# Kernel tuning notes

Measured on AMD Instinct MI355X. Metric: run time of the kernel, lower is better.

The kernel has to match this reference:

```python
import jax, jax.numpy as jnp
import numpy as np

B, S, D, H = 64, 256, 2048, 16
HD = D // H  # 128
MAXS = 256


def setup_inputs() -> dict:
    key = jax.random.key(0)
    ks = jax.random.split(key, 16)
    sc = 0.02
    inp = {
        "q": jax.random.normal(ks[0], (B, S, D), jnp.float32),
        "k": jax.random.normal(ks[1], (B, S, D), jnp.float32),
        "v": jax.random.normal(ks[2], (B, S, D), jnp.float32),
        "attention_mask": jax.random.randint(ks[3], (B, S), 0, 2, jnp.int32),
        # projection weights, torch Linear convention: y = x @ W.T + b
        "Wq": jax.random.normal(ks[4], (D, D), jnp.float32) * sc,
        "bq": jnp.zeros((D,), jnp.float32),
        "Wk": jax.random.normal(ks[5], (D, D), jnp.float32) * sc,
        "bk": jnp.zeros((D,), jnp.float32),
        "Wv": jax.random.normal(ks[6], (D, D), jnp.float32) * sc,
        "bv": jnp.zeros((D,), jnp.float32),
        "Wo": jax.random.normal(ks[7], (D, D), jnp.float32) * sc,
        "bo": jnp.zeros((D,), jnp.float32),
        # additive per-head bias table (max_sequence_length=256)
        "bias_table": jax.random.normal(ks[8], (H, MAXS, MAXS), jnp.float32) * 0.1,
    }
    return inp


def reference(q, k, v, attention_mask, Wq, bq, Wk, bk, Wv, bv, Wo, bo, bias_table):
    def proj(x, W, b):  # (B,S,D) -> (B,H,S,HD)
        y = x @ W.T + b
        return y.reshape(B, S, H, HD).transpose(0, 2, 1, 3)

    qh = proj(q, Wq, bq)
    kh = proj(k, Wk, bk)
    vh = proj(v, Wv, bv)

    # (B,H,Sq,Sk) scores
    scores = jnp.einsum("bhqd,bhkd->bhqk", qh, kh) / jnp.sqrt(jnp.float32(HD))
    scores = scores + bias_table[None, :, :S, :S]
    # mask: (B,Sk) -> (B,1,1,Sk); masked_fill where mask==0
    neg_inf = jnp.finfo(scores.dtype).min
    scores = jnp.where(attention_mask[:, None, None, :] == 0, neg_inf, scores)
    probs = jax.nn.softmax(scores, axis=-1)  # dropout p=0.0 -> identity
    out = jnp.einsum("bhqk,bhkd->bhqd", probs, vh)
    out = out.transpose(0, 2, 1, 3).reshape(B, S, D)
    return out @ Wo.T + bo
```

## Files before the change

### kernel.cpp

```cpp
#include <hip/hip_runtime.h>
#include <hip/hip_bf16.h>

typedef __attribute__((ext_vector_type(4))) float f32x4;
typedef __attribute__((ext_vector_type(8))) short s16x8;
typedef __attribute__((ext_vector_type(4))) unsigned short u16x4;
typedef __attribute__((ext_vector_type(8))) unsigned short u16x8;
typedef __attribute__((ext_vector_type(4))) int i32x4;

#define NB 64
#define NS 256
#define ND 2048
#define NH 16
#define NHD 128

__device__ __forceinline__ unsigned short f2bf(float f){
  unsigned int u = __float_as_uint(f);
  u += 0x7fffu + ((u >> 16) & 1u);
  return (unsigned short)(u >> 16);
}

__device__ __forceinline__ void gload16(const void* g, void* l){
  __builtin_amdgcn_global_load_lds(
    (const __attribute__((address_space(1))) unsigned int*)g,
    (__attribute__((address_space(3))) unsigned int*)l, 16, 0, 0);
}

#define SBAR()  __builtin_amdgcn_sched_barrier(0)
#define BARRIER() do{ SBAR(); __builtin_amdgcn_s_barrier(); SBAR(); }while(0)
#define WAIT_LGKM0() do{ asm volatile("s_waitcnt lgkmcnt(0)" ::: "memory"); SBAR(); }while(0)
#define WAIT_VM0()   do{ asm volatile("s_waitcnt vmcnt(0)"   ::: "memory"); SBAR(); }while(0)
#define WAIT_VM4()   do{ asm volatile("s_waitcnt vmcnt(4)"   ::: "memory"); SBAR(); }while(0)
#define WAIT_VM8()   do{ asm volatile("s_waitcnt vmcnt(8)"   ::: "memory"); SBAR(); }while(0)

__global__ __launch_bounds__(256) void wconv(const float* __restrict__ s,
                                             unsigned short* __restrict__ d, int n8){
  int i = blockIdx.x*256 + threadIdx.x;
  if (i >= n8) return;
  f32x4 a = *(const f32x4*)(s + (size_t)i*8);
  f32x4 b = *(const f32x4*)(s + (size_t)i*8 + 4);
  u16x8 u;
  #pragma unroll
  for (int r=0;r<4;r++){ u[r]=f2bf(a[r]); u[4+r]=f2bf(b[r]); }
  *(u16x8*)(d + (size_t)i*8) = u;
}

template<int OUTMODE>
__global__ __launch_bounds__(512, 2) void gemm256(
    const unsigned short* __restrict__ A, const unsigned short* __restrict__ Bw,
    const float* __restrict__ bias, void* __restrict__ Out, int m_base)
{
  extern __shared__ __attribute__((aligned(16))) char ldsb[];
  const int tid  = threadIdx.x;
  const int lane = tid & 63, wid = tid >> 6;
  const int g = lane >> 4, l15 = lane & 15;
  const int wm = wid >> 2, wn = wid & 3;

  const int nwg = gridDim.x, bid = blockIdx.x;
  const int swz = (bid & 7) * (nwg >> 3) + (bid >> 3);
  const int mt = swz >> 3, nt = swz & 7;
  const int m0 = mt*256, n0 = nt*256;

  const int srow_l = tid >> 3;
  const int scol   = (((tid & 7) ^ (srow_l & 7)) * 8);
  const unsigned short* gsrc[4];
  gsrc[0] = A  + (size_t)(m0 +       srow_l)*ND + scol;
  gsrc[1] = A  + (size_t)(m0 + 128 + srow_l)*ND + scol;
  gsrc[2] = Bw + (size_t)(n0 +       srow_l)*ND + scol;
  gsrc[3] = Bw + (size_t)(n0 + 128 + srow_l)*ND + scol;

#define STAGE(buf, p, kt) do{ \
    const unsigned short* s_ = gsrc[p] + (kt); \
    char* d_ = ldsb + (buf)*65536 + ((p)>>1)*32768 + ((p)&1)*16384 + tid*16; \
    gload16(s_, d_); gload16(s_ + (size_t)64*ND, d_ + 8192); }while(0)

#define RD_A(buf, qa) do{ \
    _Pragma("unroll") for (int i_=0;i_<4;i_++){ \
      int hr = (qa)*64 + i_*16 + l15; \
      const char* p_ = ldsb + (buf)*65536 + wm*16384 + hr*128; \
      _Pragma("unroll") for (int ks_=0;ks_<2;ks_++) \
        av[i_][ks_] = *(const s16x8*)(p_ + (((ks_*4+g) ^ (hr&7))*16)); } }while(0)

#define RD_B(buf, dst, qb) do{ \
    _Pragma("unroll") for (int j_=0;j_<2;j_++){ \
      int hc = (wn&1)*64 + (qb)*32 + j_*16 + l15; \
      const char* p_ = ldsb + (buf)*65536 + 32768 + (wn>>1)*16384 + hc*128; \
      _Pragma("unroll") for (int ks_=0;ks_<2;ks_++) \
        dst[j_][ks_] = *(const s16x8*)(p_ + (((ks_*4+g) ^ (hc&7))*16)); } }while(0)

#define MFMA_PH(qa, qb, bv) do{ \
    __builtin_amdgcn_s_setprio(1); \
    _Pragma("unroll") for (int i_=0;i_<4;i_++) \
      _Pragma("unroll") for (int j_=0;j_<2;j_++) \
        _Pragma("unroll") for (int ks_=0;ks_<2;ks_++) \
          acc[(qa)*4+i_][(qb)*2+j_] = __builtin_amdgcn_mfma_f32_16x16x32_bf16( \
              av[i_][ks_], bv[j_][ks_], acc[(qa)*4+i_][(qb)*2+j_], 0,0,0); \
    __builtin_amdgcn_s_setprio(0); }while(0)

#define HALF(d, ktA, ktB, wmode) do{ \
    RD_A(d,0); RD_B(d,bva,0); \
    if ((ktA)>=0) STAGE((d)^1, 0, ktA); \
    BARRIER(); WAIT_LGKM0(); \
    MFMA_PH(0,0,bva); \
    BARRIER(); \
    RD_B(d,bvb,1); \
    if ((ktA)>=0) STAGE((d)^1, 1, ktA); \
    BARRIER(); WAIT_LGKM0(); \
    MFMA_PH(0,1,bvb); \
    BARRIER(); \
    RD_A(d,1); \
    if ((ktB)>=0) STAGE(d, 2, ktB); \
    BARRIER(); WAIT_LGKM0(); \
    MFMA_PH(1,0,bva); \
    BARRIER(); \
    if ((ktB)>=0) STAGE(d, 3, ktB); \
    MFMA_PH(1,1,bvb); \
    if ((wmode)==0){ WAIT_VM4(); BARRIER(); } \
    else if ((wmode)==1){ WAIT_VM0(); BARRIER(); } \
  }while(0)

  f32x4 acc[8][4];
  s16x8 av[4][2], bva[2][2], bvb[2][2];

  STAGE(0,0,0); STAGE(0,1,0); STAGE(0,2,0); STAGE(0,3,0);
  STAGE(1,2,64); STAGE(1,3,64);
  #pragma unroll
  for (int i=0;i<8;i++)
    #pragma unroll
    for (int j=0;j<4;j++) acc[i][j] = f32x4{0.f,0.f,0.f,0.f};
  WAIT_VM4();
  BARRIER();

  for (int t = 0; t < 15; ++t) {
    HALF(0, (2*t+1)*64, (2*t+2)*64, 0);
    HALF(1, (2*t+2)*64, (2*t+3)*64, 0);
  }
  HALF(0, 31*64, -1, 1);
  HALF(1, -1, -1, -1);

  #pragma unroll
  for (int jx=0;jx<4;jx++){
    int n = n0 + wn*64 + ((jx>>1)<<5) + ((jx&1)<<4) + l15;
    float bj = bias[n];
    #pragma unroll
    for (int i=0;i<8;i++){
      int mb = m_base + m0 + wm*128 + ((i>>2)<<6) + ((i&3)<<4) + g*4;
      if (OUTMODE == 2){
        float* O = (float*)Out;
        #pragma unroll
        for (int r=0;r<4;r++) O[(size_t)(mb+r)*ND + n] = acc[i][jx][r] + bj;
      } else if (OUTMODE == 0){
        unsigned short* O = (unsigned short*)Out;
        int bb = mb >> 8, h = n >> 7, d = n & 127, s0 = mb & 255;
        #pragma unroll
        for (int r=0;r<4;r++)
          O[(((size_t)bb*NH + h)*NS + s0 + r)*NHD + d] = f2bf(acc[i][jx][r] + bj);
      } else {
        unsigned short* O = (unsigned short*)Out;
        int bb = mb >> 8, h = n >> 7, d = n & 127, s0 = mb & 255;
        u16x4 u;
        #pragma unroll
        for (int r=0;r<4;r++) u[r] = f2bf(acc[i][jx][r] + bj);
        *(u16x4*)(O + (((size_t)bb*NH + h)*NHD + d)*NS + s0) = u;
      }
    }
  }
#undef STAGE
#undef RD_A
#undef RD_B
#undef MFMA_PH
#undef HALF
}

__global__ __launch_bounds__(512, 1) void attn_fused2(
  const unsigned short* __restrict__ Qh, const unsigned short* __restrict__ Kh,
  const unsigned short* __restrict__ VT, const int* __restrict__ mask,
  const float* __restrict__ bias_table, unsigned short* __restrict__ AO)
{
  __shared__ unsigned short Klds[256*128];
  __shared__ unsigned short Vlds[128*256];
  char* Kb_ = (char*)Klds; char* Vb_ = (char*)Vlds;
  const int bh = blockIdx.x, b = bh >> 4, h = bh & 15;
  const int tid = threadIdx.x, lane = tid & 63, w = tid >> 6;
  const int g = lane >> 4, l15 = lane & 15;

  {
    const unsigned short* Ksrc = Kh + (size_t)bh*NS*NHD;
    int r0 = tid >> 4, sl = tid & 15;
    #pragma unroll
    for (int c=0;c<8;c++){
      int row = c*32 + r0;
      gload16(Ksrc + (size_t)row*NHD + ((sl ^ (row&7))*8), Kb_ + c*8192 + tid*16);
    }
  }
  {
    const unsigned short* Vsrc = VT + (size_t)bh*NHD*NS;
    int r0 = tid >> 5, sl = tid & 31;
    #pragma unroll
    for (int c=0;c<8;c++){
      int row = c*16 + r0;
      gload16(Vsrc + (size_t)row*NS + ((sl ^ (row&7))*8), Vb_ + c*8192 + tid*16);
    }
  }
  WAIT_VM8();
  BARRIER();

  const float scale = 0.08838834764831845f;
  const int* mrow = mask + b*NS;
  const int s0l = l15 + ((g&1)<<5), s1l = s0l + 16;
  const int sel = g >> 1;

  auto pass = [&](int p, bool wait_v){
    const int q = w*32 + p*16 + l15;
    const unsigned short* Qrow = Qh + ((size_t)bh*NS + q)*NHD;
    s16x8 bq[4];
    #pragma unroll
    for (int kk=0;kk<4;kk++) bq[kk] = *(const s16x8*)(Qrow + kk*32 + g*8);

    f32x4 c[16];
    __builtin_amdgcn_s_setprio(1);
    #pragma unroll
    for (int kb=0;kb<16;kb++){
      c[kb] = f32x4{0.f,0.f,0.f,0.f};
      int row = kb*16 + l15;
      #pragma unroll
      for (int kk=0;kk<4;kk++){
        s16x8 a = *(const s16x8*)(Kb_ + row*256 + (((kk*4+g) ^ (row&7))*16));
        c[kb] = __builtin_amdgcn_mfma_f32_16x16x32_bf16(a, bq[kk], c[kb], 0,0,0);
      }
    }
    __builtin_amdgcn_s_setprio(0);

    const float* brow = bias_table + ((size_t)h*NS + q)*NS;
    float mx = -3.0e38f;
    #pragma unroll
    for (int kb=0;kb<16;kb++){
      f32x4 b4 = *(const f32x4*)(brow + kb*16 + g*4);
      i32x4 m4 = *(const i32x4*)(mrow + kb*16 + g*4);
      #pragma unroll
      for (int r=0;r<4;r++){
        float val = (m4[r] != 0) ? (c[kb][r]*scale + b4[r]) : -3.0e38f;
        c[kb][r] = val;
        mx = fmaxf(mx, val);
      }
    }
    mx = fmaxf(mx, __shfl_xor(mx, 16));
    mx = fmaxf(mx, __shfl_xor(mx, 32));
    float sum = 0.f;
    #pragma unroll
    for (int kb=0;kb<16;kb++)
      #pragma unroll
      for (int r=0;r<4;r++){
        float pv = __expf(c[kb][r] - mx);
        c[kb][r] = pv; sum += pv;
      }
    sum += __shfl_xor(sum, 16);
    sum += __shfl_xor(sum, 32);
    float inv = 1.f / sum;

    unsigned int pk[16][2];
    #pragma unroll
    for (int kb=0;kb<16;kb++){
      pk[kb][0] = (unsigned int)f2bf(c[kb][0]*inv) | ((unsigned int)f2bf(c[kb][1]*inv) << 16);
      pk[kb][1] = (unsigned int)f2bf(c[kb][2]*inv) | ((unsigned int)f2bf(c[kb][3]*inv) << 16);
    }

    if (wait_v){ WAIT_VM0(); BARRIER(); }

    s16x8 pb[8];
    #pragma unroll
    for (int kk=0;kk<8;kk++){
      unsigned int e0 = (unsigned int)__shfl((int)pk[2*kk][0],   s0l);
      unsigned int e1 = (unsigned int)__shfl((int)pk[2*kk][1],   s0l);
      unsigned int e2 = (unsigned int)__shfl((int)pk[2*kk][0],   s1l);
      unsigned int e3 = (unsigned int)__shfl((int)pk[2*kk][1],   s1l);
      unsigned int o0 = (unsigned int)__shfl((int)pk[2*kk+1][0], s0l);
      unsigned int o1 = (unsigned int)__shfl((int)pk[2*kk+1][1], s0l);
      unsigned int o2 = (unsigned int)__shfl((int)pk[2*kk+1][0], s1l);
      unsigned int o3 = (unsigned int)__shfl((int)pk[2*kk+1][1], s1l);
      union { unsigned int wd[4]; s16x8 v; } u_;
      u_.wd[0] = sel ? o0 : e0; u_.wd[1] = sel ? o1 : e1;
      u_.wd[2] = sel ? o2 : e2; u_.wd[3] = sel ? o3 : e3;
      pb[kk] = u_.v;
    }

    f32x4 oacc[8];
    __builtin_amdgcn_s_setprio(1);
    #pragma unroll
    for (int dt=0;dt<8;dt++){
      oacc[dt] = f32x4{0.f,0.f,0.f,0.f};
      int row = dt*16 + l15;
      #pragma unroll
      for (int kk=0;kk<8;kk++){
        s16x8 a = *(const s16x8*)(Vb_ + row*512 + (((kk*4+g) ^ (row&7))*16));
        oacc[dt] = __builtin_amdgcn_mfma_f32_16x16x32_bf16(a, pb[kk], oacc[dt], 0,0,0);
      }
    }
    __builtin_amdgcn_s_setprio(0);

    #pragma unroll
    for (int dt=0;dt<8;dt++){
      u16x4 u;
      #pragma unroll
      for (int r=0;r<4;r++) u[r] = f2bf(oacc[dt][r]);
      *(u16x4*)(AO + ((size_t)b*NS + q)*ND + h*NHD + dt*16 + g*4) = u;
    }
  };

  pass(0, true);
  pass(1, false);
}

extern "C" void kernel_launch(void* const* d_in, const int* in_sizes, int n_in,
                              void* d_out, int out_size, void* d_ws, size_t ws_size,
                              hipStream_t stream)
{
  const float* q  = (const float*)d_in[0];
  const float* k  = (const float*)d_in[1];
  const float* v  = (const float*)d_in[2];
  const int* mask = (const int*)d_in[3];
  const float* Wq = (const float*)d_in[4];
  const float* bq = (const float*)d_in[5];
  const float* Wk = (const float*)d_in[6];
  const float* bk = (const float*)d_in[7];
  const float* Wv = (const float*)d_in[8];
  const float* bv = (const float*)d_in[9];
  const float* Wo = (const float*)d_in[10];
  const float* bo = (const float*)d_in[11];
  const float* bias_table = (const float*)d_in[12];

  char* ws = (char*)d_ws;
  unsigned short* Wob = (unsigned short*)(ws + 0);
  unsigned short* wb  = (unsigned short*)(ws + 8388608);
  unsigned short* tmp = (unsigned short*)(ws + 16777216);
  unsigned short* Qh  = (unsigned short*)(ws + 83886080);
  unsigned short* Kh  = (unsigned short*)(ws + 150994944);
  unsigned short* VT  = (unsigned short*)(ws + 218103808);
  unsigned short* AO  = (unsigned short*)(ws + 285212672);

  hipFuncSetAttribute((const void*)gemm256<0>, hipFuncAttributeMaxDynamicSharedMemorySize, 131072);
  hipFuncSetAttribute((const void*)gemm256<1>, hipFuncAttributeMaxDynamicSharedMemorySize, 131072);
  hipFuncSetAttribute((const void*)gemm256<2>, hipFuncAttributeMaxDynamicSharedMemorySize, 131072);

  wconv<<<2048,256,0,stream>>>(Wo, Wob, 524288);

  const float* acts[3]  = {q, k, v};
  const float* wgt[3]   = {Wq, Wk, Wv};
  const float* bia[3]   = {bq, bk, bv};
  unsigned short* outs[3] = {Qh, Kh, VT};

  for (int x = 0; x < 3; ++x) {
    wconv<<<2048,256,0,stream>>>(wgt[x], wb, 524288);
    wconv<<<16384,256,0,stream>>>(acts[x], tmp, 4194304);
    if (x < 2)
      gemm256<0><<<512,512,131072,stream>>>(tmp, wb, bia[x], outs[x], 0);
    else
      gemm256<1><<<512,512,131072,stream>>>(tmp, wb, bia[x], outs[x], 0);
  }

  attn_fused2<<<1024,512,0,stream>>>(Qh,Kh,VT,mask,bias_table,AO);
  gemm256<2><<<512,512,131072,stream>>>(AO,Wob,bo,(float*)d_out,0);
}
```

Before: 745.6 us.

## Fuse fp32-to-bf16 activation conversion into the QKV projection GEMM loads

Adds a GEMM variant that loads fp32 activations straight into registers, converts them to bf16 and writes them to LDS inside the software pipeline, replacing the separate activation conversion kernels and their scratch buffer. This removes three full-size fp32 read plus bf16 write/read round trips through memory. In exchange the A-operand staging now goes through registers rather than direct global-to-LDS loads, which raises register pressure and adds conversion ALU work inside the main loop. Weight conversions are also hoisted into four back-to-back launches up front.

```diff
diff --git a/kernel.cpp b/kernel.cpp
--- a/kernel.cpp
+++ b/kernel.cpp
@@ -44,34 +44,17 @@
   *(u16x8*)(d + (size_t)i*8) = u;
 }
 
-template<int OUTMODE>
-__global__ __launch_bounds__(512, 2) void gemm256(
-    const unsigned short* __restrict__ A, const unsigned short* __restrict__ Bw,
-    const float* __restrict__ bias, void* __restrict__ Out, int m_base)
-{
-  extern __shared__ __attribute__((aligned(16))) char ldsb[];
-  const int tid  = threadIdx.x;
-  const int lane = tid & 63, wid = tid >> 6;
-  const int g = lane >> 4, l15 = lane & 15;
-  const int wm = wid >> 2, wn = wid & 3;
-
-  const int nwg = gridDim.x, bid = blockIdx.x;
-  const int swz = (bid & 7) * (nwg >> 3) + (bid >> 3);
-  const int mt = swz >> 3, nt = swz & 7;
-  const int m0 = mt*256, n0 = nt*256;
-
-  const int srow_l = tid >> 3;
-  const int scol   = (((tid & 7) ^ (srow_l & 7)) * 8);
-  const unsigned short* gsrc[4];
-  gsrc[0] = A  + (size_t)(m0 +       srow_l)*ND + scol;
-  gsrc[1] = A  + (size_t)(m0 + 128 + srow_l)*ND + scol;
-  gsrc[2] = Bw + (size_t)(n0 +       srow_l)*ND + scol;
-  gsrc[3] = Bw + (size_t)(n0 + 128 + srow_l)*ND + scol;
-
-#define STAGE(buf, p, kt) do{ \
-    const unsigned short* s_ = gsrc[p] + (kt); \
-    char* d_ = ldsb + (buf)*65536 + ((p)>>1)*32768 + ((p)&1)*16384 + tid*16; \
-    gload16(s_, d_); gload16(s_ + (size_t)64*ND, d_ + 8192); }while(0)
+#define GEMM_COMMON_DECLS \
+  extern __shared__ __attribute__((aligned(16))) char ldsb[]; \
+  const int tid  = threadIdx.x; \
+  const int lane = tid & 63, wid = tid >> 6; \
+  const int g = lane >> 4, l15 = lane & 15; \
+  const int wm = wid >> 2, wn = wid & 3; \
+  const int nwg = gridDim.x, bid = blockIdx.x; \
+  const int swz = (bid & 7) * (nwg >> 3) + (bid >> 3); \
+  const int mt = swz >> 3, nt = swz & 7; \
+  const int m0 = mt*256, n0 = nt*256; \
+  const int srow_l = tid >> 3, slot = tid & 7;
 
 #define RD_A(buf, qa) do{ \
     _Pragma("unroll") for (int i_=0;i_<4;i_++){ \
@@ -96,6 +79,50 @@
               av[i_][ks_], bv[j_][ks_], acc[(qa)*4+i_][(qb)*2+j_], 0,0,0); \
     __builtin_amdgcn_s_setprio(0); }while(0)
 
+#define GEMM_EPILOGUE(OUTMODE_) \
+  _Pragma("unroll") \
+  for (int jx=0;jx<4;jx++){ \
+    int n = n0 + wn*64 + ((jx>>1)<<5) + ((jx&1)<<4) + l15; \
+    float bj = bias[n]; \
+    _Pragma("unroll") \
+    for (int i=0;i<8;i++){ \
+      int mb = m0 + wm*128 + ((i>>2)<<6) + ((i&3)<<4) + g*4; \
+      if ((OUTMODE_) == 2){ \
+        float* O = (float*)Out; \
+        _Pragma("unroll") for (int r=0;r<4;r++) O[(size_t)(mb+r)*ND + n] = acc[i][jx][r] + bj; \
+      } else if ((OUTMODE_) == 0){ \
+        unsigned short* O = (unsigned short*)Out; \
+        int bb = mb >> 8, h = n >> 7, d = n & 127, s0 = mb & 255; \
+        _Pragma("unroll") for (int r=0;r<4;r++) \
+          O[(((size_t)bb*NH + h)*NS + s0 + r)*NHD + d] = f2bf(acc[i][jx][r] + bj); \
+      } else { \
+        unsigned short* O = (unsigned short*)Out; \
+        int bb = mb >> 8, h = n >> 7, d = n & 127, s0 = mb & 255; \
+        u16x4 u; \
+        _Pragma("unroll") for (int r=0;r<4;r++) u[r] = f2bf(acc[i][jx][r] + bj); \
+        *(u16x4*)(O + (((size_t)bb*NH + h)*NHD + d)*NS + s0) = u; \
+      } \
+    } \
+  }
+
+template<int OUTMODE>
+__global__ __launch_bounds__(512, 2) void gemm256(
+    const unsigned short* __restrict__ A, const unsigned short* __restrict__ Bw,
+    const float* __restrict__ bias, void* __restrict__ Out)
+{
+  GEMM_COMMON_DECLS
+  const int scol = ((slot ^ (srow_l & 7)) * 8);
+  const unsigned short* gsrc[4];
+  gsrc[0] = A  + (size_t)(m0 +       srow_l)*ND + scol;
+  gsrc[1] = A  + (size_t)(m0 + 128 + srow_l)*ND + scol;
+  gsrc[2] = Bw + (size_t)(n0 +       srow_l)*ND + scol;
+  gsrc[3] = Bw + (size_t)(n0 + 128 + srow_l)*ND + scol;
+
+#define STAGE(buf, p, kt) do{ \
+    const unsigned short* s_ = gsrc[p] + (kt); \
+    char* d_ = ldsb + (buf)*65536 + ((p)>>1)*32768 + ((p)&1)*16384 + tid*16; \
+    gload16(s_, d_); gload16(s_ + (size_t)64*ND, d_ + 8192); }while(0)
+
 #define HALF(d, ktA, ktB, wmode) do{ \
     RD_A(d,0); RD_B(d,bva,0); \
     if ((ktA)>=0) STAGE((d)^1, 0, ktA); \
@@ -137,38 +164,94 @@
   HALF(0, 31*64, -1, 1);
   HALF(1, -1, -1, -1);
 
+  GEMM_EPILOGUE(OUTMODE)
+#undef STAGE
+#undef HALF
+}
+
+template<int OUTMODE>
+__global__ __launch_bounds__(512, 2) void gemm256f(
+    const float* __restrict__ Af, const unsigned short* __restrict__ Bw,
+    const float* __restrict__ bias, void* __restrict__ Out)
+{
+  GEMM_COMMON_DECLS
+  const int scol = ((slot ^ (srow_l & 7)) * 8);
+  const unsigned short* gsrcB[2];
+  gsrcB[0] = Bw + (size_t)(n0 +       srow_l)*ND + scol;
+  gsrcB[1] = Bw + (size_t)(n0 + 128 + srow_l)*ND + scol;
+  const int swA = (srow_l*8 + (slot ^ (srow_l & 7)))*16;
+
+#define STAGEB(buf, p, kt) do{ \
+    const unsigned short* s_ = gsrcB[p] + (kt); \
+    char* d_ = ldsb + (buf)*65536 + 32768 + (p)*16384 + tid*16; \
+    gload16(s_, d_); gload16(s_ + (size_t)64*ND, d_ + 8192); }while(0)
+
+#define STAGE_A_LOAD(p, kt, X) do{ \
+    const float* s_ = Af + (size_t)(m0 + (p)*128 + srow_l)*ND + (kt) + slot*8; \
+    X[0] = *(const f32x4*)(s_);               X[1] = *(const f32x4*)(s_ + 4); \
+    X[2] = *(const f32x4*)(s_ + (size_t)64*ND); X[3] = *(const f32x4*)(s_ + (size_t)64*ND + 4); }while(0)
+
+#define STAGE_A_WRITE(buf, p, X) do{ \
+    u16x8 u0_, u1_; \
+    _Pragma("unroll") for (int r_=0;r_<4;r_++){ \
+      u0_[r_]=f2bf(X[0][r_]); u0_[4+r_]=f2bf(X[1][r_]); \
+      u1_[r_]=f2bf(X[2][r_]); u1_[4+r_]=f2bf(X[3][r_]); } \
+    char* w_ = ldsb + (buf)*65536 + (p)*16384 + swA; \
+    *(u16x8*)(w_) = u0_; *(u16x8*)(w_ + 8192) = u1_; }while(0)
+
+#define HALFF(d, ktA, ktB, wmode) do{ \
+    RD_A(d,0); RD_B(d,bva,0); \
+    if ((ktA)>=0) STAGE_A_LOAD(0, ktA, XA); \
+    BARRIER(); WAIT_LGKM0(); \
+    MFMA_PH(0,0,bva); \
+    BARRIER(); \
+    RD_B(d,bvb,1); \
+    if ((ktA)>=0) STAGE_A_LOAD(1, ktA, XB); \
+    BARRIER(); WAIT_LGKM0(); \
+    MFMA_PH(0,1,bvb); \
+    BARRIER(); \
+    RD_A(d,1); \
+    if ((ktB)>=0) STAGEB(d, 0, ktB); \
+    BARRIER(); WAIT_LGKM0(); \
+    MFMA_PH(1,0,bva); \
+    BARRIER(); \
+    if ((ktB)>=0) STAGEB(d, 1, ktB); \
+    if ((wmode)==0) WAIT_VM4(); \
+    else if ((wmode)==1) WAIT_VM0(); \
+    if ((ktA)>=0){ STAGE_A_WRITE((d)^1, 0, XA); STAGE_A_WRITE((d)^1, 1, XB); } \
+    MFMA_PH(1,1,bvb); \
+    WAIT_LGKM0(); \
+    BARRIER(); \
+  }while(0)
+
+  f32x4 acc[8][4];
+  f32x4 XA[4], XB[4];
+  s16x8 av[4][2], bva[2][2], bvb[2][2];
+
+  STAGE_A_LOAD(0, 0, XA); STAGE_A_LOAD(1, 0, XB);
+  STAGEB(0,0,0); STAGEB(0,1,0);
+  STAGEB(1,0,64); STAGEB(1,1,64);
   #pragma unroll
-  for (int jx=0;jx<4;jx++){
-    int n = n0 + wn*64 + ((jx>>1)<<5) + ((jx&1)<<4) + l15;
-    float bj = bias[n];
-    #pragma unroll
-    for (int i=0;i<8;i++){
-      int mb = m_base + m0 + wm*128 + ((i>>2)<<6) + ((i&3)<<4) + g*4;
-      if (OUTMODE == 2){
-        float* O = (float*)Out;
-        #pragma unroll
-        for (int r=0;r<4;r++) O[(size_t)(mb+r)*ND + n] = acc[i][jx][r] + bj;
-      } else if (OUTMODE == 0){
-        unsigned short* O = (unsigned short*)Out;
-        int bb = mb >> 8, h = n >> 7, d = n & 127, s0 = mb & 255;
-        #pragma unroll
-        for (int r=0;r<4;r++)
-          O[(((size_t)bb*NH + h)*NS + s0 + r)*NHD + d] = f2bf(acc[i][jx][r] + bj);
-      } else {
-        unsigned short* O = (unsigned short*)Out;
-        int bb = mb >> 8, h = n >> 7, d = n & 127, s0 = mb & 255;
-        u16x4 u;
-        #pragma unroll
-        for (int r=0;r<4;r++) u[r] = f2bf(acc[i][jx][r] + bj);
-        *(u16x4*)(O + (((size_t)bb*NH + h)*NHD + d)*NS + s0) = u;
-      }
-    }
+  for (int i=0;i<8;i++)
+    #pragma unroll
+    for (int j=0;j<4;j++) acc[i][j] = f32x4{0.f,0.f,0.f,0.f};
+  WAIT_VM4();
+  STAGE_A_WRITE(0,0,XA); STAGE_A_WRITE(0,1,XB);
+  WAIT_LGKM0();
+  BARRIER();
+
+  for (int t = 0; t < 15; ++t) {
+    HALFF(0, (2*t+1)*64, (2*t+2)*64, 0);
+    HALFF(1, (2*t+2)*64, (2*t+3)*64, 0);
   }
-#undef STAGE
-#undef RD_A
-#undef RD_B
-#undef MFMA_PH
-#undef HALF
+  HALFF(0, 31*64, -1, 1);
+  HALFF(1, -1, -1, 2);
+
+  GEMM_EPILOGUE(OUTMODE)
+#undef STAGEB
+#undef STAGE_A_LOAD
+#undef STAGE_A_WRITE
+#undef HALFF
 }
 
 __global__ __launch_bounds__(512, 1) void attn_fused2(
@@ -329,34 +412,28 @@
   const float* bias_table = (const float*)d_in[12];
 
   char* ws = (char*)d_ws;
-  unsigned short* Wob = (unsigned short*)(ws + 0);
-  unsigned short* wb  = (unsigned short*)(ws + 8388608);
-  unsigned short* tmp = (unsigned short*)(ws + 16777216);
-  unsigned short* Qh  = (unsigned short*)(ws + 83886080);
-  unsigned short* Kh  = (unsigned short*)(ws + 150994944);
-  unsigned short* VT  = (unsigned short*)(ws + 218103808);
-  unsigned short* AO  = (unsigned short*)(ws + 285212672);
-
-  hipFuncSetAttribute((const void*)gemm256<0>, hipFuncAttributeMaxDynamicSharedMemorySize, 131072);
-  hipFuncSetAttribute((const void*)gemm256<1>, hipFuncAttributeMaxDynamicSharedMemorySize, 131072);
-  hipFuncSetAttribute((const void*)gemm256<2>, hipFuncAttributeMaxDynamicSharedMemorySize, 131072);
-
+  unsigned short* Wqb = (unsigned short*)(ws + 0);
+  unsigned short* Wkb = (unsigned short*)(ws + 8388608);
+  unsigned short* Wvb = (unsigned short*)(ws + 16777216);
+  unsigned short* Wob = (unsigned short*)(ws + 25165824);
+  unsigned short* Qh  = (unsigned short*)(ws + 33554432);
+  unsigned short* Kh  = (unsigned short*)(ws + 100663296);
+  unsigned short* VT  = (unsigned short*)(ws + 167772160);
+  unsigned short* AO  = (unsigned short*)(ws + 234881024);
+
+  hipFuncSetAttribute((const void*)gemm256f<0>, hipFuncAttributeMaxDynamicSharedMemorySize, 131072);
+  hipFuncSetAttribute((const void*)gemm256f<1>, hipFuncAttributeMaxDynamicSharedMemorySize, 131072);
+  hipFuncSetAttribute((const void*)gemm256<2>,  hipFuncAttributeMaxDynamicSharedMemorySize, 131072);
+
+  wconv<<<2048,256,0,stream>>>(Wq, Wqb, 524288);
+  wconv<<<2048,256,0,stream>>>(Wk, Wkb, 524288);
+  wconv<<<2048,256,0,stream>>>(Wv, Wvb, 524288);
   wconv<<<2048,256,0,stream>>>(Wo, Wob, 524288);
 
-  const float* acts[3]  = {q, k, v};
-  const float* wgt[3]   = {Wq, Wk, Wv};
-  const float* bia[3]   = {bq, bk, bv};
-  unsigned short* outs[3] = {Qh, Kh, VT};
-
-  for (int x = 0; x < 3; ++x) {
-    wconv<<<2048,256,0,stream>>>(wgt[x], wb, 524288);
-    wconv<<<16384,256,0,stream>>>(acts[x], tmp, 4194304);
-    if (x < 2)
-      gemm256<0><<<512,512,131072,stream>>>(tmp, wb, bia[x], outs[x], 0);
-    else
-      gemm256<1><<<512,512,131072,stream>>>(tmp, wb, bia[x], outs[x], 0);
-  }
+  gemm256f<0><<<512,512,131072,stream>>>(q, Wqb, bq, Qh);
+  gemm256f<0><<<512,512,131072,stream>>>(k, Wkb, bk, Kh);
+  gemm256f<1><<<512,512,131072,stream>>>(v, Wvb, bv, VT);
 
   attn_fused2<<<1024,512,0,stream>>>(Qh,Kh,VT,mask,bias_table,AO);
-  gemm256<2><<<512,512,131072,stream>>>(AO,Wob,bo,(float*)d_out,0);
-}
+  gemm256<2><<<512,512,131072,stream>>>(AO,Wob,bo,(float*)d_out);
+}
```

Result: slower. 853.3 us (+14.4%).
